# Optimization experiments

Measured on AMD Instinct MI355X. Metric: run time of the kernel, lower is better.

## Reference

```python
import jax, jax.numpy as jnp
import numpy as np

# irrep multiplicities (match init_kwargs)
M0E, M1O, M1E, M0O = 64, 32, 32, 16
IN_DIM = M0E + 3 * M1O + 3 * M1E + M0O  # 272
# weight block shapes, in the fixed key order 0e, 1o, 1e, 0o
W_SHAPES = [("0e", M0E + M1O, M0E), ("1o", M0E + M1O + M1E, M1O), ("1e", M1O + M1E + M0O, M1E), ("0o", M1E + M0O, M0O)]
W_NUMEL = sum(a * b for _, a, b in W_SHAPES)  # 13568


def setup_inputs() -> dict:
    key = jax.random.key(0)
    k1, k2, k3 = jax.random.split(key, 3)
    B, N = 4, 128
    return {
        "in_": jax.random.normal(k1, (B, 1, N, IN_DIM), dtype=jnp.float32),
        "sh": jax.random.normal(k2, (B, N, 1, 4), dtype=jnp.float32),
        "weight": jax.random.normal(k3, (W_NUMEL,), dtype=jnp.float32),
    }


def _split_weights(weight):
    out, start = {}, 0
    for key, a, b in W_SHAPES:
        out[key] = weight[..., start:start + a * b].reshape(weight.shape[:-1] + (a, b)) / np.sqrt(a).astype(np.float32)
        start += a * b
    return out


def reference(in_, sh, weight):
    # split input irreps: [B,1,N,272] -> 0e [B,1,N,64], 1o [B,1,N,32,3], 1e [B,1,N,32,3], 0o [B,1,N,16]
    i = 0
    x0e = in_[..., i:i + M0E]; i += M0E
    x1o = in_[..., i:i + 3 * M1O].reshape(in_.shape[:-1] + (M1O, 3)); i += 3 * M1O
    x1e = in_[..., i:i + 3 * M1E].reshape(in_.shape[:-1] + (M1E, 3)); i += 3 * M1E
    x0o = in_[..., i:i + M0O]

    sh0 = sh[..., 0]          # [B,N,1]
    sh1 = sh[..., 1:]         # [B,N,1,3]
    sh1b = sh1[..., None, :]  # [B,N,1,1,3] (broadcast against mul axis)
    inv_s3 = np.float32(1.0 / np.sqrt(3.0))
    inv_s2 = np.float32(1.0 / np.sqrt(2.0))

    # pairwise broadcast: [B,1,N,...] x [B,N,1,...] -> [B,N,N,...]
    out0e = jnp.concatenate([
        x0e * sh0[..., None],                       # [B,N,N,64]
        (x1o * sh1b).sum(-1) * inv_s3,              # [B,N,N,32]
    ], axis=-1)                                     # [B,N,N,96]

    out1o = jnp.concatenate([
        x0e[..., None] * sh1b,                      # [B,N,N,64,3]
        x1o * sh0[..., None, None],                 # [B,N,N,32,3]
        jnp.cross(x1e, sh1b) * inv_s2,              # [B,N,N,32,3]
    ], axis=-2)                                     # [B,N,N,128,3]

    out1e = jnp.concatenate([
        jnp.cross(x1o, sh1b) * inv_s2,              # [B,N,N,32,3]
        x1e * sh0[..., None, None],                 # [B,N,N,32,3]
        x0o[..., None] * sh1b,                      # [B,N,N,16,3]
    ], axis=-2)                                     # [B,N,N,80,3]

    out0o = jnp.concatenate([
        (x1e * sh1b).sum(-1) * inv_s3,              # [B,N,N,32]
        x0o * sh0[..., None],                       # [B,N,N,16]
    ], axis=-1)                                     # [B,N,N,48]

    W = _split_weights(weight)
    y0e = out0e @ W["0e"]                                            # [B,N,N,64]
    y1o = jnp.einsum("bnmkc,ko->bnmoc", out1o, W["1o"])             # [B,N,N,32,3]
    y1o = y1o.reshape(y1o.shape[:-2] + (-1,))                        # [B,N,N,96]
    y1e = jnp.einsum("bnmkc,ko->bnmoc", out1e, W["1e"])             # [B,N,N,32,3]
    y1e = y1e.reshape(y1e.shape[:-2] + (-1,))                        # [B,N,N,96]
    y0o = out0o @ W["0o"]                                            # [B,N,N,16]

    # out_irreps order: 64x0e + 32x1o + 32x1e + 16x0o
    return jnp.concatenate([y0e, y1o, y1e, y0o], axis=-1)            # [B,N,N,272]
```

## Files before the change

kernel.cpp:

```cpp
#include <hip/hip_runtime.h>


constexpr float INV_S3 = 0.57735026918962576f;
constexpr float INV_S2 = 0.70710678118654752f;
constexpr float SC0E = 0.10206207261596577f;
constexpr float SC1O = 0.08838834764831845f;
constexpr float SC1E = 0.11180339887498949f;
constexpr float SC0O = 0.14433756729740643f;

#define P0E 97
#define P1O 129
#define P1E 81
#define P0O 49

__global__ __launch_bounds__(320) void stage_a(const float* __restrict__ in_,
                                               const float* __restrict__ weight,
                                               float* __restrict__ Z) {
    __shared__ float xs[272];
    __shared__ float o0e[4 * P0E];
    __shared__ float o1oT[12 * P1O];
    __shared__ float o1eT[12 * P1E];
    __shared__ float o0o[4 * P0O];

    const int tid = threadIdx.x;
    const int row = blockIdx.x;
    const float* x = in_ + row * 272;

    if (tid < 68) ((float4*)xs)[tid] = ((const float4*)x)[tid];
    __syncthreads();

    for (int idx = tid; idx < 4 * 96; idx += 320) {
        int c = idx / 96, k = idx - c * 96;
        float v = 0.f;
        if (k < 64) { if (c == 0) v = xs[k]; }
        else        { if (c >= 1) v = xs[64 + (k - 64) * 3 + (c - 1)] * INV_S3; }
        o0e[c * P0E + k] = v * SC0E;
    }
    for (int idx = tid; idx < 4 * 3 * 128; idx += 320) {
        int c = idx / 384, rem = idx - c * 384, d = rem >> 7, k = rem & 127;
        float v = 0.f;
        if (k < 64) {
            if (c >= 1 && d == c - 1) v = xs[k];
        } else if (k < 96) {
            if (c == 0) v = xs[64 + (k - 64) * 3 + d];
        } else {
            if (c >= 1) {
                int t = c - 1, j = k - 96;
                float a1 = xs[160 + j * 3 + (d + 1) % 3];
                float a2 = xs[160 + j * 3 + (d + 2) % 3];
                v = ((((d + 2) % 3) == t) ? a1 : 0.f) - ((((d + 1) % 3) == t) ? a2 : 0.f);
                v *= INV_S2;
            }
        }
        o1oT[(c * 3 + d) * P1O + k] = v * SC1O;
    }
    for (int idx = tid; idx < 4 * 3 * 80; idx += 320) {
        int c = idx / 240, rem = idx - c * 240, d = rem / 80, k = rem - d * 80;
        float v = 0.f;
        if (k < 32) {
            if (c >= 1) {
                int t = c - 1;
                float a1 = xs[64 + k * 3 + (d + 1) % 3];
                float a2 = xs[64 + k * 3 + (d + 2) % 3];
                v = ((((d + 2) % 3) == t) ? a1 : 0.f) - ((((d + 1) % 3) == t) ? a2 : 0.f);
                v *= INV_S2;
            }
        } else if (k < 64) {
            if (c == 0) v = xs[160 + (k - 32) * 3 + d];
        } else {
            if (c >= 1 && d == c - 1) v = xs[256 + (k - 64)];
        }
        o1eT[(c * 3 + d) * P1E + k] = v * SC1E;
    }
    for (int idx = tid; idx < 4 * 48; idx += 320) {
        int c = idx / 48, k = idx - c * 48;
        float v = 0.f;
        if (k < 32) { if (c >= 1) v = xs[160 + k * 3 + (c - 1)] * INV_S3; }
        else        { if (c == 0) v = xs[256 + (k - 32)]; }
        o0o[c * P0O + k] = v * SC0O;
    }
    __syncthreads();

    float* zrow = Z + row * 1088;

    if (tid < 64) {
        int c = tid >> 4, o4 = tid & 15;
        const float* wp = weight + o4 * 4;
        const float* op = o0e + c * P0E;
        float ax = 0.f, ay = 0.f, az = 0.f, aw = 0.f;
        #pragma unroll 8
        for (int k = 0; k < 96; ++k) {
            float s = op[k];
            float4 w = *(const float4*)(wp + k * 64);
            ax += s * w.x; ay += s * w.y; az += s * w.z; aw += s * w.w;
        }
        float4 r; r.x = ax; r.y = ay; r.z = az; r.w = aw;
        *(float4*)(zrow + c * 272 + o4 * 4) = r;
    } else if (tid < 160) {
        int t2 = tid - 64;
        int c = t2 / 24, r2 = t2 - c * 24, d = r2 >> 3, o4 = r2 & 7;
        const float* wp = weight + 6144 + o4 * 4;
        const float* op = o1oT + (c * 3 + d) * P1O;
        float ax = 0.f, ay = 0.f, az = 0.f, aw = 0.f;
        #pragma unroll 8
        for (int k = 0; k < 128; ++k) {
            float s = op[k];
            float4 w = *(const float4*)(wp + k * 32);
            ax += s * w.x; ay += s * w.y; az += s * w.z; aw += s * w.w;
        }
        float* zb = zrow + c * 272 + 64 + d;
        zb[(o4 * 4 + 0) * 3] = ax;
        zb[(o4 * 4 + 1) * 3] = ay;
        zb[(o4 * 4 + 2) * 3] = az;
        zb[(o4 * 4 + 3) * 3] = aw;
    } else if (tid < 256) {
        int t2 = tid - 160;
        int c = t2 / 24, r2 = t2 - c * 24, d = r2 >> 3, o4 = r2 & 7;
        const float* wp = weight + 10240 + o4 * 4;
        const float* op = o1eT + (c * 3 + d) * P1E;
        float ax = 0.f, ay = 0.f, az = 0.f, aw = 0.f;
        #pragma unroll 8
        for (int k = 0; k < 80; ++k) {
            float s = op[k];
            float4 w = *(const float4*)(wp + k * 32);
            ax += s * w.x; ay += s * w.y; az += s * w.z; aw += s * w.w;
        }
        float* zb = zrow + c * 272 + 160 + d;
        zb[(o4 * 4 + 0) * 3] = ax;
        zb[(o4 * 4 + 1) * 3] = ay;
        zb[(o4 * 4 + 2) * 3] = az;
        zb[(o4 * 4 + 3) * 3] = aw;
    } else if (tid < 272) {
        int t2 = tid - 256;
        int c = t2 >> 2, o4 = t2 & 3;
        const float* wp = weight + 12800 + o4 * 4;
        const float* op = o0o + c * P0O;
        float ax = 0.f, ay = 0.f, az = 0.f, aw = 0.f;
        #pragma unroll 8
        for (int k = 0; k < 48; ++k) {
            float s = op[k];
            float4 w = *(const float4*)(wp + k * 16);
            ax += s * w.x; ay += s * w.y; az += s * w.z; aw += s * w.w;
        }
        float4 r; r.x = ax; r.y = ay; r.z = az; r.w = aw;
        *(float4*)(zrow + c * 272 + 256 + o4 * 4) = r;
    }
}

__global__ __launch_bounds__(256) void stage_b(const float4* __restrict__ Z4,
                                               const float4* __restrict__ sh4,
                                               float4* __restrict__ out4) {
    int g = blockIdx.x * 256 + threadIdx.x;
    int bm = g / 8704;
    int p  = g - bm * 8704;
    int n  = p / 68;
    int o4 = p - n * 68;
    int b  = bm >> 7;

    float4 s = sh4[bm];
    const float4* zr = Z4 + (size_t)((b * 128 + n) * 4) * 68 + o4;
    float4 z0 = zr[0];
    float4 z1 = zr[68];
    float4 z2 = zr[2 * 68];
    float4 z3 = zr[3 * 68];

    float4 v;
    v.x = s.x * z0.x + s.y * z1.x + s.z * z2.x + s.w * z3.x;
    v.y = s.x * z0.y + s.y * z1.y + s.z * z2.y + s.w * z3.y;
    v.z = s.x * z0.z + s.y * z1.z + s.z * z2.z + s.w * z3.z;
    v.w = s.x * z0.w + s.y * z1.w + s.z * z2.w + s.w * z3.w;
    out4[g] = v;
}

extern "C" void kernel_launch(void* const* d_in, const int* in_sizes, int n_in,
                              void* d_out, int out_size, void* d_ws, size_t ws_size,
                              hipStream_t stream) {
    (void)in_sizes; (void)n_in; (void)out_size; (void)ws_size;
    const float* in_ = (const float*)d_in[0];
    const float* sh  = (const float*)d_in[1];
    const float* w   = (const float*)d_in[2];
    float* Z = (float*)d_ws;
    float* out = (float*)d_out;

    stage_a<<<512, 320, 0, stream>>>(in_, w, Z);
    stage_b<<<17408, 256, 0, stream>>>((const float4*)Z, (const float4*)sh, (float4*)out);
}
```

Before: 104.3 us.

## Fuse weight contraction and sh broadcast into one kernel via shared memory

Merges the two kernels: each block computes its row's four Z vectors into shared memory, then broadcasts them against all 128 sh entries, writing output directly. This removes the global workspace write/read and one launch. In exchange, output writes come from only 512 blocks with 272 active threads each looping over 32 strided stores, which may underutilize memory bandwidth compared to the massively parallel previous second stage.

```diff
diff --git a/kernel.cpp b/kernel.cpp
--- a/kernel.cpp
+++ b/kernel.cpp
@@ -13,30 +13,35 @@
 #define P1E 81
 #define P0O 49
 
-__global__ __launch_bounds__(320) void stage_a(const float* __restrict__ in_,
-                                               const float* __restrict__ weight,
-                                               float* __restrict__ Z) {
+__global__ __launch_bounds__(384) void fused_tp(const float* __restrict__ in_,
+                                                const float* __restrict__ weight,
+                                                const float4* __restrict__ sh4,
+                                                float4* __restrict__ out4) {
     __shared__ float xs[272];
     __shared__ float o0e[4 * P0E];
     __shared__ float o1oT[12 * P1O];
     __shared__ float o1eT[12 * P1E];
     __shared__ float o0o[4 * P0O];
+    __shared__ float4 zs4[272];
+    float* zs = (float*)zs4;
 
     const int tid = threadIdx.x;
     const int row = blockIdx.x;
+    const int b = row >> 7;
+    const int n = row & 127;
     const float* x = in_ + row * 272;
 
     if (tid < 68) ((float4*)xs)[tid] = ((const float4*)x)[tid];
     __syncthreads();
 
-    for (int idx = tid; idx < 4 * 96; idx += 320) {
+    for (int idx = tid; idx < 4 * 96; idx += 384) {
         int c = idx / 96, k = idx - c * 96;
         float v = 0.f;
         if (k < 64) { if (c == 0) v = xs[k]; }
         else        { if (c >= 1) v = xs[64 + (k - 64) * 3 + (c - 1)] * INV_S3; }
         o0e[c * P0E + k] = v * SC0E;
     }
-    for (int idx = tid; idx < 4 * 3 * 128; idx += 320) {
+    for (int idx = tid; idx < 4 * 3 * 128; idx += 384) {
         int c = idx / 384, rem = idx - c * 384, d = rem >> 7, k = rem & 127;
         float v = 0.f;
         if (k < 64) {
@@ -54,7 +59,7 @@
         }
         o1oT[(c * 3 + d) * P1O + k] = v * SC1O;
     }
-    for (int idx = tid; idx < 4 * 3 * 80; idx += 320) {
+    for (int idx = tid; idx < 4 * 3 * 80; idx += 384) {
         int c = idx / 240, rem = idx - c * 240, d = rem / 80, k = rem - d * 80;
         float v = 0.f;
         if (k < 32) {
@@ -72,7 +77,7 @@
         }
         o1eT[(c * 3 + d) * P1E + k] = v * SC1E;
     }
-    for (int idx = tid; idx < 4 * 48; idx += 320) {
+    for (int idx = tid; idx < 4 * 48; idx += 384) {
         int c = idx / 48, k = idx - c * 48;
         float v = 0.f;
         if (k < 32) { if (c >= 1) v = xs[160 + k * 3 + (c - 1)] * INV_S3; }
@@ -81,10 +86,10 @@
     }
     __syncthreads();
 
-    float* zrow = Z + row * 1088;
+    const int wave = tid >> 6, lane = tid & 63;
 
-    if (tid < 64) {
-        int c = tid >> 4, o4 = tid & 15;
+    if (wave == 0) {
+        int c = lane >> 4, o4 = lane & 15;
         const float* wp = weight + o4 * 4;
         const float* op = o0e + c * P0E;
         float ax = 0.f, ay = 0.f, az = 0.f, aw = 0.f;
@@ -95,93 +100,92 @@
             ax += s * w.x; ay += s * w.y; az += s * w.z; aw += s * w.w;
         }
         float4 r; r.x = ax; r.y = ay; r.z = az; r.w = aw;
-        *(float4*)(zrow + c * 272 + o4 * 4) = r;
-    } else if (tid < 160) {
-        int t2 = tid - 64;
-        int c = t2 / 24, r2 = t2 - c * 24, d = r2 >> 3, o4 = r2 & 7;
-        const float* wp = weight + 6144 + o4 * 4;
-        const float* op = o1oT + (c * 3 + d) * P1O;
-        float ax = 0.f, ay = 0.f, az = 0.f, aw = 0.f;
-        #pragma unroll 8
-        for (int k = 0; k < 128; ++k) {
-            float s = op[k];
-            float4 w = *(const float4*)(wp + k * 32);
-            ax += s * w.x; ay += s * w.y; az += s * w.z; aw += s * w.w;
+        *(float4*)(zs + c * 272 + o4 * 4) = r;
+    } else if (wave == 1 || wave == 2) {
+        int t2 = (wave == 1) ? lane : 64 + lane;
+        if (t2 < 96) {
+            int c = t2 / 24, r2 = t2 - c * 24, d = r2 >> 3, o4 = r2 & 7;
+            const float* wp = weight + 6144 + o4 * 4;
+            const float* op = o1oT + (c * 3 + d) * P1O;
+            float ax = 0.f, ay = 0.f, az = 0.f, aw = 0.f;
+            #pragma unroll 8
+            for (int k = 0; k < 128; ++k) {
+                float s = op[k];
+                float4 w = *(const float4*)(wp + k * 32);
+                ax += s * w.x; ay += s * w.y; az += s * w.z; aw += s * w.w;
+            }
+            float* zb = zs + c * 272 + 64 + d;
+            zb[(o4 * 4 + 0) * 3] = ax;
+            zb[(o4 * 4 + 1) * 3] = ay;
+            zb[(o4 * 4 + 2) * 3] = az;
+            zb[(o4 * 4 + 3) * 3] = aw;
         }
-        float* zb = zrow + c * 272 + 64 + d;
-        zb[(o4 * 4 + 0) * 3] = ax;
-        zb[(o4 * 4 + 1) * 3] = ay;
-        zb[(o4 * 4 + 2) * 3] = az;
-        zb[(o4 * 4 + 3) * 3] = aw;
-    } else if (tid < 256) {
-        int t2 = tid - 160;
-        int c = t2 / 24, r2 = t2 - c * 24, d = r2 >> 3, o4 = r2 & 7;
-        const float* wp = weight + 10240 + o4 * 4;
-        const float* op = o1eT + (c * 3 + d) * P1E;
-        float ax = 0.f, ay = 0.f, az = 0.f, aw = 0.f;
-        #pragma unroll 8
-        for (int k = 0; k < 80; ++k) {
-            float s = op[k];
-            float4 w = *(const float4*)(wp + k * 32);
-            ax += s * w.x; ay += s * w.y; az += s * w.z; aw += s * w.w;
+    } else if (wave == 3 || wave == 4) {
+        int t2 = (wave == 3) ? lane : 64 + lane;
+        if (t2 < 96) {
+            int c = t2 / 24, r2 = t2 - c * 24, d = r2 >> 3, o4 = r2 & 7;
+            const float* wp = weight + 10240 + o4 * 4;
+            const float* op = o1eT + (c * 3 + d) * P1E;
+            float ax = 0.f, ay = 0.f, az = 0.f, aw = 0.f;
+            #pragma unroll 8
+            for (int k = 0; k < 80; ++k) {
+                float s = op[k];
+                float4 w = *(const float4*)(wp + k * 32);
+                ax += s * w.x; ay += s * w.y; az += s * w.z; aw += s * w.w;
+            }
+            float* zb = zs + c * 272 + 160 + d;
+            zb[(o4 * 4 + 0) * 3] = ax;
+            zb[(o4 * 4 + 1) * 3] = ay;
+            zb[(o4 * 4 + 2) * 3] = az;
+            zb[(o4 * 4 + 3) * 3] = aw;
         }
-        float* zb = zrow + c * 272 + 160 + d;
-        zb[(o4 * 4 + 0) * 3] = ax;
-        zb[(o4 * 4 + 1) * 3] = ay;
-        zb[(o4 * 4 + 2) * 3] = az;
-        zb[(o4 * 4 + 3) * 3] = aw;
-    } else if (tid < 272) {
-        int t2 = tid - 256;
-        int c = t2 >> 2, o4 = t2 & 3;
-        const float* wp = weight + 12800 + o4 * 4;
-        const float* op = o0o + c * P0O;
-        float ax = 0.f, ay = 0.f, az = 0.f, aw = 0.f;
-        #pragma unroll 8
-        for (int k = 0; k < 48; ++k) {
-            float s = op[k];
-            float4 w = *(const float4*)(wp + k * 16);
-            ax += s * w.x; ay += s * w.y; az += s * w.z; aw += s * w.w;
+    } else {
+        if (lane < 16) {
+            int c = lane >> 2, o4 = lane & 3;
+            const float* wp = weight + 12800 + o4 * 4;
+            const float* op = o0o + c * P0O;
+            float ax = 0.f, ay = 0.f, az = 0.f, aw = 0.f;
+            #pragma unroll 8
+            for (int k = 0; k < 48; ++k) {
+                float s = op[k];
+                float4 w = *(const float4*)(wp + k * 16);
+                ax += s * w.x; ay += s * w.y; az += s * w.z; aw += s * w.w;
+            }
+            float4 r; r.x = ax; r.y = ay; r.z = az; r.w = aw;
+            *(float4*)(zs + c * 272 + 256 + o4 * 4) = r;
         }
-        float4 r; r.x = ax; r.y = ay; r.z = az; r.w = aw;
-        *(float4*)(zrow + c * 272 + 256 + o4 * 4) = r;
     }
-}
+    __syncthreads();
 
-__global__ __launch_bounds__(256) void stage_b(const float4* __restrict__ Z4,
-                                               const float4* __restrict__ sh4,
-                                               float4* __restrict__ out4) {
-    int g = blockIdx.x * 256 + threadIdx.x;
-    int bm = g / 8704;
-    int p  = g - bm * 8704;
-    int n  = p / 68;
-    int o4 = p - n * 68;
-    int b  = bm >> 7;
-
-    float4 s = sh4[bm];
-    const float4* zr = Z4 + (size_t)((b * 128 + n) * 4) * 68 + o4;
-    float4 z0 = zr[0];
-    float4 z1 = zr[68];
-    float4 z2 = zr[2 * 68];
-    float4 z3 = zr[3 * 68];
-
-    float4 v;
-    v.x = s.x * z0.x + s.y * z1.x + s.z * z2.x + s.w * z3.x;
-    v.y = s.x * z0.y + s.y * z1.y + s.z * z2.y + s.w * z3.y;
-    v.z = s.x * z0.z + s.y * z1.z + s.z * z2.z + s.w * z3.z;
-    v.w = s.x * z0.w + s.y * z1.w + s.z * z2.w + s.w * z3.w;
-    out4[g] = v;
+    if (tid < 272) {
+        int mq = tid / 68, o4 = tid - mq * 68;
+        float4 z0 = zs4[0 * 68 + o4];
+        float4 z1 = zs4[1 * 68 + o4];
+        float4 z2 = zs4[2 * 68 + o4];
+        float4 z3 = zs4[3 * 68 + o4];
+        const float4* shp = sh4 + (b << 7) + mq * 32;
+        float4* ob = out4 + ((size_t)((b << 7) + mq * 32) * 8704) + n * 68 + o4;
+        #pragma unroll 4
+        for (int it = 0; it < 32; ++it) {
+            float4 s = shp[it];
+            float4 v;
+            v.x = s.x * z0.x + s.y * z1.x + s.z * z2.x + s.w * z3.x;
+            v.y = s.x * z0.y + s.y * z1.y + s.z * z2.y + s.w * z3.y;
+            v.z = s.x * z0.z + s.y * z1.z + s.z * z2.z + s.w * z3.z;
+            v.w = s.x * z0.w + s.y * z1.w + s.z * z2.w + s.w * z3.w;
+            ob[(size_t)it * 8704] = v;
+        }
+    }
 }
 
 extern "C" void kernel_launch(void* const* d_in, const int* in_sizes, int n_in,
                               void* d_out, int out_size, void* d_ws, size_t ws_size,
                               hipStream_t stream) {
-    (void)in_sizes; (void)n_in; (void)out_size; (void)ws_size;
+    (void)in_sizes; (void)n_in; (void)out_size; (void)d_ws; (void)ws_size;
     const float* in_ = (const float*)d_in[0];
     const float* sh  = (const float*)d_in[1];
     const float* w   = (const float*)d_in[2];
-    float* Z = (float*)d_ws;
-    float* out = (float*)d_out;
+    float4* out = (float4*)d_out;
 
-    stage_a<<<512, 320, 0, stream>>>(in_, w, Z);
-    stage_b<<<17408, 256, 0, stream>>>((const float4*)Z, (const float4*)sh, (float4*)out);
+    fused_tp<<<512, 384, 0, stream>>>(in_, w, (const float4*)sh, out);
 }
```

New measurement: 107.6 us. +3.2%, slower.
